# Optimization experiments

Measured on AMD Instinct MI355X. Metric: run time of the kernel, lower is better.

Reference implementation:

```python
import jax, jax.numpy as jnp
import numpy as np
from jax.scipy.special import logsumexp

B = 4096        # batch_size
D = 512         # feature dim
C = 128         # class_num
TEMP_F = 0.5
TEMP_L = 1.0
LAMBDA1 = 0.5
LAMBDA2 = 0.5
COS_EPS = 1e-8  # torch CosineSimilarity eps


def setup_inputs() -> dict:
    key = jax.random.key(0)
    k1, k2, k3, k4, k5 = jax.random.split(key, 5)
    return {
        "h1": jax.random.normal(k1, (B, D), dtype=jnp.float32),
        "h2": jax.random.normal(k2, (B, D), dtype=jnp.float32),
        "q1": jax.random.uniform(k3, (B, C), dtype=jnp.float32),
        "q2": jax.random.uniform(k4, (B, C), dtype=jnp.float32),
        "confidence": jax.random.uniform(k5, (B,), dtype=jnp.float32),
    }


def _ntxent_from_sim(sim, half):
    """NT-Xent per-row loss given full sim matrix [2*half, 2*half].

    Key identity: logits row r = [pos_r, negatives_r] where negatives exclude
    cols {r, partner(r)} and pos_r = sim[r, partner(r)]. Hence
    CE(logits, 0) = logsumexp over row excluding only the diagonal, minus pos.
    """
    N = 2 * half
    pos = jnp.concatenate([jnp.diagonal(sim, offset=half),
                           jnp.diagonal(sim, offset=-half)], axis=0)  # [N]
    eye = jnp.eye(N, dtype=bool)
    sim_masked = jnp.where(eye, -jnp.inf, sim)
    lse = logsumexp(sim_masked, axis=1)  # [N]
    return lse - pos  # per-row CE loss


def _forward_feature(h_i, h_j, confidence):
    b = h_i.shape[0]
    h = jnp.concatenate([h_i, h_j], axis=0)              # [2B, D]
    sim = jnp.matmul(h, h.T) / TEMP_F                     # [2B, 2B]
    loss = _ntxent_from_sim(sim, b)                       # [2B]
    loss = loss * jnp.tile(confidence, 2)                 # confidence.repeat(2)
    return loss.mean()


def _forward_label(q_i, q_j):
    c = q_i.shape[1]
    p_i = q_i.sum(0)
    p_i = p_i / p_i.sum()
    ne_i = jnp.log(jnp.float32(c)) + (p_i * jnp.log(p_i)).sum()
    p_j = q_j.sum(0)
    p_j = p_j / p_j.sum()
    ne_j = jnp.log(jnp.float32(c)) + (p_j * jnp.log(p_j)).sum()
    entropy = ne_i + ne_j

    q = jnp.concatenate([q_i.T, q_j.T], axis=0)           # [2C, B]
    norms = jnp.linalg.norm(q, axis=1)                    # [2C]
    denom = jnp.maximum(norms[:, None] * norms[None, :], COS_EPS)
    sim = (q @ q.T) / denom / TEMP_L                      # [2C, 2C]
    loss = _ntxent_from_sim(sim, c)                       # [2C]
    return loss.mean() + entropy


def reference(h1, h2, q1, q2, confidence):
    loss_feat = _forward_feature(h1, h2, confidence)
    loss_label = _forward_label(q1, q2)
    return LAMBDA1 * loss_feat + LAMBDA2 * loss_label
```

## Files before the change

kernel.cpp:

```cpp
#include <hip/hip_runtime.h>

typedef __attribute__((ext_vector_type(8))) short short8;
typedef __attribute__((ext_vector_type(4))) float f32x4;

#define NROW 8192
#define D_SZ 512

#define HB_OFF     0u
#define SPARTL_OFF 0u
#define SGRAM_OFF  2097152u
#define PSUMP_OFF  2359296u
#define FPART_OFF  2363392u
#define POS_OFF    8388608u
#define MPART_OFF  8421376u
#define SPARTF_OFF 8683520u

__device__ __forceinline__ unsigned short f32_to_bf16(float f) {
  unsigned int u = __float_as_uint(f);
  u = (u + 0x7FFFu + ((u >> 16) & 1u)) >> 16;
  return (unsigned short)u;
}

__global__ void convert_kernel(const float* __restrict__ h1, const float* __restrict__ h2,
                               unsigned short* __restrict__ hb) {
  int tid = blockIdx.x * 256 + threadIdx.x;
  float4 v = (tid < 524288) ? reinterpret_cast<const float4*>(h1)[tid]
                            : reinterpret_cast<const float4*>(h2)[tid - 524288];
  ushort4 o;
  o.x = f32_to_bf16(v.x); o.y = f32_to_bf16(v.y);
  o.z = f32_to_bf16(v.z); o.w = f32_to_bf16(v.w);
  reinterpret_cast<ushort4*>(hb)[tid] = o;
}

__global__ __launch_bounds__(256, 2) void feature_kernel(
    const short* __restrict__ hb, float* __restrict__ pos,
    float* __restrict__ mpart, float* __restrict__ spart) {
  __shared__ short lds_s[32 * 512];
  const int tid = threadIdx.x;
  const int w = tid >> 6;
  const int lane = tid & 63;
  const int lo16 = lane & 15;
  const int grp = lane >> 4;
  const int cz = blockIdx.x;
  const int bt = blockIdx.y;
  const int Rw = bt * 128 + w * 32;

  short8 A[2][16];
#pragma unroll
  for (int rt = 0; rt < 2; ++rt) {
    const short* ab = hb + (Rw + rt * 16 + lo16) * D_SZ + grp * 8;
#pragma unroll
    for (int kk = 0; kk < 16; ++kk)
      A[rt][kk] = *reinterpret_cast<const short8*>(ab + kk * 32);
  }
#pragma unroll
  for (int rt = 0; rt < 2; ++rt)
#pragma unroll
    for (int kk = 0; kk < 16; ++kk)
      asm volatile("" : "+v"(A[rt][kk]));

  float m0 = -INFINITY, m1 = -INFINITY, s0 = 0.f, s1 = 0.f;
  const int r0 = Rw + lo16;
  const int r1 = Rw + 16 + lo16;
  const int p0 = (r0 + 4096) & 8191;
  const int p1 = (r1 + 4096) & 8191;
  const int swz = (lo16 & 7) << 3;

#pragma unroll 1
  for (int g = 0; g < 32; ++g) {
    const int cg = cz * 1024 + g * 32;
    __syncthreads();
#pragma unroll
    for (int i = 0; i < 8; ++i) {
      int ch = i * 256 + tid;
      int col = ch >> 6, k8 = ch & 63;
      short8 v = *reinterpret_cast<const short8*>(hb + (cg + col) * D_SZ + k8 * 8);
      int dst = col * D_SZ + ((k8 * 8) ^ ((col & 7) << 3));
      *reinterpret_cast<short8*>(&lds_s[dst]) = v;
    }
    __syncthreads();

    f32x4 acc00 = {0,0,0,0}, acc01 = {0,0,0,0}, acc10 = {0,0,0,0}, acc11 = {0,0,0,0};
#pragma unroll
    for (int kk = 0; kk < 16; ++kk) {
      const int k = kk * 32 + grp * 8;
      short8 B0 = *reinterpret_cast<const short8*>(&lds_s[lo16 * D_SZ + (k ^ swz)]);
      short8 B1 = *reinterpret_cast<const short8*>(&lds_s[(16 + lo16) * D_SZ + (k ^ swz)]);
      acc00 = __builtin_amdgcn_mfma_f32_16x16x32_bf16(B0, A[0][kk], acc00, 0, 0, 0);
      acc01 = __builtin_amdgcn_mfma_f32_16x16x32_bf16(B0, A[1][kk], acc01, 0, 0, 0);
      acc10 = __builtin_amdgcn_mfma_f32_16x16x32_bf16(B1, A[0][kk], acc10, 0, 0, 0);
      acc11 = __builtin_amdgcn_mfma_f32_16x16x32_bf16(B1, A[1][kk], acc11, 0, 0, 0);
    }

    const int cbase = cg + grp * 4;
    {
      float v[8];
#pragma unroll
      for (int j = 0; j < 4; ++j) { v[j] = acc00[j] * 2.f; v[4 + j] = acc10[j] * 2.f; }
#pragma unroll
      for (int j = 0; j < 4; ++j) {
        int c0 = cbase + j, c1 = cbase + 16 + j;
        if (c0 == p0) pos[r0] = v[j];
        if (c1 == p0) pos[r0] = v[4 + j];
        if (c0 == r0) v[j] = -INFINITY;
        if (c1 == r0) v[4 + j] = -INFINITY;
      }
      float tm = v[0];
#pragma unroll
      for (int i = 1; i < 8; ++i) tm = fmaxf(tm, v[i]);
      tm = fmaxf(tm, __shfl_xor(tm, 16));
      tm = fmaxf(tm, __shfl_xor(tm, 32));
      float mn = fmaxf(m0, tm);
      float e = 0.f;
#pragma unroll
      for (int i = 0; i < 8; ++i) e += __expf(v[i] - mn);
      e += __shfl_xor(e, 16);
      e += __shfl_xor(e, 32);
      s0 = s0 * __expf(m0 - mn) + e;
      m0 = mn;
    }
    {
      float v[8];
#pragma unroll
      for (int j = 0; j < 4; ++j) { v[j] = acc01[j] * 2.f; v[4 + j] = acc11[j] * 2.f; }
#pragma unroll
      for (int j = 0; j < 4; ++j) {
        int c0 = cbase + j, c1 = cbase + 16 + j;
        if (c0 == p1) pos[r1] = v[j];
        if (c1 == p1) pos[r1] = v[4 + j];
        if (c0 == r1) v[j] = -INFINITY;
        if (c1 == r1) v[4 + j] = -INFINITY;
      }
      float tm = v[0];
#pragma unroll
      for (int i = 1; i < 8; ++i) tm = fmaxf(tm, v[i]);
      tm = fmaxf(tm, __shfl_xor(tm, 16));
      tm = fmaxf(tm, __shfl_xor(tm, 32));
      float mn = fmaxf(m1, tm);
      float e = 0.f;
#pragma unroll
      for (int i = 0; i < 8; ++i) e += __expf(v[i] - mn);
      e += __shfl_xor(e, 16);
      e += __shfl_xor(e, 32);
      s1 = s1 * __expf(m1 - mn) + e;
      m1 = mn;
    }
  }

  if (grp == 0) {
    mpart[cz * NROW + r0] = m0; spart[cz * NROW + r0] = s0;
    mpart[cz * NROW + r1] = m1; spart[cz * NROW + r1] = s1;
  }
}

__global__ void combine_feature_kernel(const float* __restrict__ mpart,
                                       const float* __restrict__ spart,
                                       const float* __restrict__ pos,
                                       const float* __restrict__ conf,
                                       float* __restrict__ fpart) {
  __shared__ float red[256];
  int r = blockIdx.x * 256 + threadIdx.x;
  float M = -INFINITY;
#pragma unroll
  for (int k = 0; k < 8; ++k) M = fmaxf(M, mpart[k * NROW + r]);
  float S = 0.f;
#pragma unroll
  for (int k = 0; k < 8; ++k) S += spart[k * NROW + r] * __expf(mpart[k * NROW + r] - M);
  float lse = logf(S) + M;
  float loss = (lse - pos[r]) * conf[r & 4095];
  red[threadIdx.x] = loss;
  __syncthreads();
  for (int s = 128; s > 0; s >>= 1) {
    if (threadIdx.x < s) red[threadIdx.x] += red[threadIdx.x + s];
    __syncthreads();
  }
  if (threadIdx.x == 0) fpart[blockIdx.x] = red[0];
}

__global__ __launch_bounds__(256) void label_gemm_kernel(const float* __restrict__ q1,
                                                         const float* __restrict__ q2,
                                                         float* __restrict__ Spart) {
  __shared__ float As[32 * 64];
  __shared__ float Bs[32 * 32];
  const int t = threadIdx.x;
  const int kz = blockIdx.x >> 5;
  const int bi = (blockIdx.x & 31) >> 3;
  const int bj = blockIdx.x & 7;
  const int tx = t & 15, ty = t >> 4;
  float a[4][2];
#pragma unroll
  for (int dr = 0; dr < 4; ++dr)
#pragma unroll
    for (int dc = 0; dc < 2; ++dc) a[dr][dc] = 0.f;

  for (int ch = 0; ch < 16; ++ch) {
    const int kbase = kz * 512 + ch * 32;
    __syncthreads();
#pragma unroll
    for (int i = 0; i < 8; ++i) {
      int e = i * 256 + t;
      int kr = e >> 6, j = e & 63;
      int ca = bi * 64 + j;
      As[kr * 64 + j] = (ca < 128) ? q1[(kbase + kr) * 128 + ca]
                                   : q2[(kbase + kr) * 128 + ca - 128];
    }
#pragma unroll
    for (int i = 0; i < 4; ++i) {
      int e = i * 256 + t;
      int kr = e >> 5, j = e & 31;
      int cb = bj * 32 + j;
      Bs[kr * 32 + j] = (cb < 128) ? q1[(kbase + kr) * 128 + cb]
                                   : q2[(kbase + kr) * 128 + cb - 128];
    }
    __syncthreads();
#pragma unroll 8
    for (int k = 0; k < 32; ++k) {
      float4 Av = *reinterpret_cast<const float4*>(&As[k * 64 + ty * 4]);
      float2 Bv = *reinterpret_cast<const float2*>(&Bs[k * 32 + tx * 2]);
      a[0][0] += Av.x * Bv.x; a[0][1] += Av.x * Bv.y;
      a[1][0] += Av.y * Bv.x; a[1][1] += Av.y * Bv.y;
      a[2][0] += Av.z * Bv.x; a[2][1] += Av.z * Bv.y;
      a[3][0] += Av.w * Bv.x; a[3][1] += Av.w * Bv.y;
    }
  }
  float* outp = Spart + kz * 65536;
#pragma unroll
  for (int dr = 0; dr < 4; ++dr) {
    int r = bi * 64 + ty * 4 + dr;
    int c = bj * 32 + tx * 2;
    outp[r * 256 + c] = a[dr][0];
    outp[r * 256 + c + 1] = a[dr][1];
  }
}

__global__ void label_prep_kernel(const float* __restrict__ q1, const float* __restrict__ q2,
                                  const float* __restrict__ Spart, float* __restrict__ S,
                                  float* __restrict__ psum_part) {
  const int b = blockIdx.x, t = threadIdx.x;
  if (b < 256) {
    int e = b * 256 + t;
    float acc = 0.f;
#pragma unroll
    for (int kz = 0; kz < 8; ++kz) acc += Spart[kz * 65536 + e];
    S[e] = acc;
  } else {
    __shared__ float sd[256];
    int idx = b - 256;
    const float* q = (idx < 4) ? q1 : q2;
    int col = t & 127, half = t >> 7;
    int rbase = (idx & 3) * 1024 + half * 512;
    float acc = 0.f;
    for (int i = 0; i < 512; ++i) acc += q[(rbase + i) * 128 + col];
    sd[t] = acc;
    __syncthreads();
    if (t < 128) psum_part[idx * 128 + col] = sd[t] + sd[t + 128];
  }
}

__global__ __launch_bounds__(256) void label_final_kernel(
    const float* __restrict__ S, const float* __restrict__ psum_part,
    const float* __restrict__ fpart, float* __restrict__ out) {
  __shared__ float nrm[256], red[256], redl[256];
  __shared__ float entropy_sh, feat_sh;
  const int t = threadIdx.x;
  nrm[t] = sqrtf(fmaxf(S[t * 257], 0.f));
  const float* pp = psum_part + (t >> 7) * 512 + (t & 127);
  float v = pp[0] + pp[128] + pp[256] + pp[384];
  red[t] = v;
  redl[t] = v * logf(fmaxf(v, 1e-30f));
  __syncthreads();
  for (int s = 64; s > 0; s >>= 1) {
    if ((t & 127) < s) { red[t] += red[t + s]; redl[t] += redl[t + s]; }
    __syncthreads();
  }
  if (t == 0) {
    float tot1 = red[0], tot2 = red[128];
    float ne1 = logf(128.f) + (redl[0] / tot1 - logf(tot1));
    float ne2 = logf(128.f) + (redl[128] / tot2 - logf(tot2));
    entropy_sh = ne1 + ne2;
  }
  __syncthreads();
  red[t] = (t < 32) ? fpart[t] : 0.f;
  __syncthreads();
  for (int s = 128; s > 0; s >>= 1) {
    if (t < s) red[t] += red[t + s];
    __syncthreads();
  }
  if (t == 0) feat_sh = red[0];
  __syncthreads();

  const float nr = nrm[t];
  const float* Srow = S + t * 256;
  const int partner = (t + 128) & 255;
  float m = -INFINITY;
  for (int c = 0; c < 256; ++c) {
    if (c == t) continue;
    float sv = Srow[c] / fmaxf(nr * nrm[c], 1e-8f);
    m = fmaxf(m, sv);
  }
  float ssum = 0.f, posv = 0.f;
  for (int c = 0; c < 256; ++c) {
    float sv = Srow[c] / fmaxf(nr * nrm[c], 1e-8f);
    if (c == partner) posv = sv;
    if (c != t) ssum += __expf(sv - m);
  }
  float loss_r = (logf(ssum) + m) - posv;
  __syncthreads();
  red[t] = loss_r;
  __syncthreads();
  for (int s = 128; s > 0; s >>= 1) {
    if (t < s) red[t] += red[t + s];
    __syncthreads();
  }
  if (t == 0)
    out[0] = 0.5f * (feat_sh / 8192.f) + 0.5f * (red[0] / 256.f + entropy_sh);
}

extern "C" void kernel_launch(void* const* d_in, const int* in_sizes, int n_in,
                              void* d_out, int out_size, void* d_ws, size_t ws_size,
                              hipStream_t stream) {
  const float* h1 = (const float*)d_in[0];
  const float* h2 = (const float*)d_in[1];
  const float* q1 = (const float*)d_in[2];
  const float* q2 = (const float*)d_in[3];
  const float* conf = (const float*)d_in[4];
  float* out = (float*)d_out;
  char* ws = (char*)d_ws;

  unsigned short* hb = (unsigned short*)(ws + HB_OFF);
  float* pos    = (float*)(ws + POS_OFF);
  float* mpart  = (float*)(ws + MPART_OFF);
  float* spartf = (float*)(ws + SPARTF_OFF);
  float* SpartL = (float*)(ws + SPARTL_OFF);
  float* Sgram  = (float*)(ws + SGRAM_OFF);
  float* psump  = (float*)(ws + PSUMP_OFF);
  float* fpart  = (float*)(ws + FPART_OFF);

  convert_kernel<<<4096, 256, 0, stream>>>(h1, h2, hb);
  feature_kernel<<<dim3(8, 64), 256, 0, stream>>>((const short*)hb, pos, mpart, spartf);
  combine_feature_kernel<<<32, 256, 0, stream>>>(mpart, spartf, pos, conf, fpart);
  label_gemm_kernel<<<256, 256, 0, stream>>>(q1, q2, SpartL);
  label_prep_kernel<<<264, 256, 0, stream>>>(q1, q2, SpartL, Sgram, psump);
  label_final_kernel<<<1, 256, 0, stream>>>(Sgram, psump, fpart, out);
}
```

Baseline: 272.9 us.

## Double-buffer B tiles via direct global-to-LDS loads and defer cross-lane softmax reduction

Replaces the register-staged, twice-synchronized B tile load with asynchronous global_load_lds into a double-buffered LDS array, prefetching the next 32-column tile while the current one is multiplied. The swizzle is now applied on the global address side so the LDS layout stays compatible. The per-iteration cross-lane max/sum shuffles are dropped: each lane keeps its own online-softmax state, and states are merged with shuffles once after the loop. This doubles LDS use per block, which may affect occupancy, and relies on correct ordering of the async LDS writes with a single barrier per iteration.

```diff
diff --git a/kernel.cpp b/kernel.cpp
--- a/kernel.cpp
+++ b/kernel.cpp
@@ -14,6 +14,11 @@
 #define POS_OFF    8388608u
 #define MPART_OFF  8421376u
 #define SPARTF_OFF 8683520u
+
+#define GLOAD_LDS(gp, lp)                                     \
+  __builtin_amdgcn_global_load_lds(                           \
+      (const __attribute__((address_space(1))) void*)(gp),    \
+      (__attribute__((address_space(3))) void*)(lp), 16, 0, 0)
 
 __device__ __forceinline__ unsigned short f32_to_bf16(float f) {
   unsigned int u = __float_as_uint(f);
@@ -35,7 +40,7 @@
 __global__ __launch_bounds__(256, 2) void feature_kernel(
     const short* __restrict__ hb, float* __restrict__ pos,
     float* __restrict__ mpart, float* __restrict__ spart) {
-  __shared__ short lds_s[32 * 512];
+  __shared__ short lds_s[2][16384];
   const int tid = threadIdx.x;
   const int w = tid >> 6;
   const int lane = tid & 63;
@@ -53,11 +58,24 @@
     for (int kk = 0; kk < 16; ++kk)
       A[rt][kk] = *reinterpret_cast<const short8*>(ab + kk * 32);
   }
-#pragma unroll
-  for (int rt = 0; rt < 2; ++rt)
-#pragma unroll
-    for (int kk = 0; kk < 16; ++kk)
-      asm volatile("" : "+v"(A[rt][kk]));
+
+  const short* p_even = hb + (cz * 1024 + w) * D_SZ + (lane ^ w) * 8;
+  const short* p_odd  = hb + (cz * 1024 + w) * D_SZ + (lane ^ (w + 4)) * 8;
+  short* ldbase = &lds_s[0][tid * 8];
+
+#define STAGE(g, b) do {                                   \
+    const short* pe_ = p_even + (g) * 16384;               \
+    const short* po_ = p_odd + (g) * 16384;                \
+    short* ld_ = ldbase + (b) * 16384;                     \
+    GLOAD_LDS(pe_, ld_);                                   \
+    GLOAD_LDS(po_ + 2048, ld_ + 2048);                     \
+    GLOAD_LDS(pe_ + 4096, ld_ + 4096);                     \
+    GLOAD_LDS(po_ + 6144, ld_ + 6144);                     \
+    GLOAD_LDS(pe_ + 8192, ld_ + 8192);                     \
+    GLOAD_LDS(po_ + 10240, ld_ + 10240);                   \
+    GLOAD_LDS(pe_ + 12288, ld_ + 12288);                   \
+    GLOAD_LDS(po_ + 14336, ld_ + 14336);                   \
+  } while (0)
 
   float m0 = -INFINITY, m1 = -INFINITY, s0 = 0.f, s1 = 0.f;
   const int r0 = Rw + lo16;
@@ -66,33 +84,34 @@
   const int p1 = (r1 + 4096) & 8191;
   const int swz = (lo16 & 7) << 3;
 
+  STAGE(0, 0);
+  __syncthreads();
+
 #pragma unroll 1
   for (int g = 0; g < 32; ++g) {
-    const int cg = cz * 1024 + g * 32;
-    __syncthreads();
-#pragma unroll
-    for (int i = 0; i < 8; ++i) {
-      int ch = i * 256 + tid;
-      int col = ch >> 6, k8 = ch & 63;
-      short8 v = *reinterpret_cast<const short8*>(hb + (cg + col) * D_SZ + k8 * 8);
-      int dst = col * D_SZ + ((k8 * 8) ^ ((col & 7) << 3));
-      *reinterpret_cast<short8*>(&lds_s[dst]) = v;
-    }
-    __syncthreads();
-
+    const int cur = g & 1;
+    if (g < 31) STAGE(g + 1, cur ^ 1);
+
+#pragma unroll
+    for (int rt = 0; rt < 2; ++rt)
+#pragma unroll
+      for (int kk = 0; kk < 16; ++kk)
+        asm volatile("" : "+v"(A[rt][kk]));
+
+    const short* bufp = &lds_s[cur][0];
     f32x4 acc00 = {0,0,0,0}, acc01 = {0,0,0,0}, acc10 = {0,0,0,0}, acc11 = {0,0,0,0};
 #pragma unroll
     for (int kk = 0; kk < 16; ++kk) {
       const int k = kk * 32 + grp * 8;
-      short8 B0 = *reinterpret_cast<const short8*>(&lds_s[lo16 * D_SZ + (k ^ swz)]);
-      short8 B1 = *reinterpret_cast<const short8*>(&lds_s[(16 + lo16) * D_SZ + (k ^ swz)]);
+      short8 B0 = *reinterpret_cast<const short8*>(&bufp[lo16 * D_SZ + (k ^ swz)]);
+      short8 B1 = *reinterpret_cast<const short8*>(&bufp[(16 + lo16) * D_SZ + (k ^ swz)]);
       acc00 = __builtin_amdgcn_mfma_f32_16x16x32_bf16(B0, A[0][kk], acc00, 0, 0, 0);
       acc01 = __builtin_amdgcn_mfma_f32_16x16x32_bf16(B0, A[1][kk], acc01, 0, 0, 0);
       acc10 = __builtin_amdgcn_mfma_f32_16x16x32_bf16(B1, A[0][kk], acc10, 0, 0, 0);
       acc11 = __builtin_amdgcn_mfma_f32_16x16x32_bf16(B1, A[1][kk], acc11, 0, 0, 0);
     }
 
-    const int cbase = cg + grp * 4;
+    const int cbase = cz * 1024 + g * 32 + grp * 4;
     {
       float v[8];
 #pragma unroll
@@ -105,17 +124,12 @@
         if (c0 == r0) v[j] = -INFINITY;
         if (c1 == r0) v[4 + j] = -INFINITY;
       }
-      float tm = v[0];
-#pragma unroll
-      for (int i = 1; i < 8; ++i) tm = fmaxf(tm, v[i]);
-      tm = fmaxf(tm, __shfl_xor(tm, 16));
-      tm = fmaxf(tm, __shfl_xor(tm, 32));
+      float tm = fmaxf(fmaxf(fmaxf(v[0], v[1]), fmaxf(v[2], v[3])),
+                       fmaxf(fmaxf(v[4], v[5]), fmaxf(v[6], v[7])));
       float mn = fmaxf(m0, tm);
       float e = 0.f;
 #pragma unroll
       for (int i = 0; i < 8; ++i) e += __expf(v[i] - mn);
-      e += __shfl_xor(e, 16);
-      e += __shfl_xor(e, 32);
       s0 = s0 * __expf(m0 - mn) + e;
       m0 = mn;
     }
@@ -131,26 +145,36 @@
         if (c0 == r1) v[j] = -INFINITY;
         if (c1 == r1) v[4 + j] = -INFINITY;
       }
-      float tm = v[0];
-#pragma unroll
-      for (int i = 1; i < 8; ++i) tm = fmaxf(tm, v[i]);
-      tm = fmaxf(tm, __shfl_xor(tm, 16));
-      tm = fmaxf(tm, __shfl_xor(tm, 32));
+      float tm = fmaxf(fmaxf(fmaxf(v[0], v[1]), fmaxf(v[2], v[3])),
+                       fmaxf(fmaxf(v[4], v[5]), fmaxf(v[6], v[7])));
       float mn = fmaxf(m1, tm);
       float e = 0.f;
 #pragma unroll
       for (int i = 0; i < 8; ++i) e += __expf(v[i] - mn);
-      e += __shfl_xor(e, 16);
-      e += __shfl_xor(e, 32);
       s1 = s1 * __expf(m1 - mn) + e;
       m1 = mn;
     }
+
+    __syncthreads();
+  }
+
+#pragma unroll
+  for (int off = 16; off <= 32; off <<= 1) {
+    float mo = __shfl_xor(m0, off), so = __shfl_xor(s0, off);
+    float mn = fmaxf(m0, mo);
+    s0 = s0 * __expf(m0 - mn) + so * __expf(mo - mn);
+    m0 = mn;
+    mo = __shfl_xor(m1, off); so = __shfl_xor(s1, off);
+    mn = fmaxf(m1, mo);
+    s1 = s1 * __expf(m1 - mn) + so * __expf(mo - mn);
+    m1 = mn;
   }
 
   if (grp == 0) {
     mpart[cz * NROW + r0] = m0; spart[cz * NROW + r0] = s0;
     mpart[cz * NROW + r1] = m1; spart[cz * NROW + r1] = s1;
   }
+#undef STAGE
 }
 
 __global__ void combine_feature_kernel(const float* __restrict__ mpart,
```

After: 269.1 us. Within noise of the previous version (-1.4%).
